# Kernel optimization log

Hardware: AMD Instinct MI355X
Metric: run time of the kernel (lower is better)

## Reference

```python
import jax, jax.numpy as jnp
import numpy as np
from jax import lax

SEQ, BATCH, IN, HID = 4096, 8, 1024, 1024


def setup_inputs() -> dict:
    key = jax.random.key(0)
    k1, k2 = jax.random.split(key)
    X = jax.random.normal(k1, (SEQ, BATCH, IN), dtype=jnp.float32)
    hidden = jnp.zeros((BATCH, HID), dtype=jnp.float32)  # None init == zeros
    W = jax.random.normal(k2, (3 * HID, IN), dtype=jnp.float32) * 0.02
    b = jnp.zeros((3 * HID,), dtype=jnp.float32)
    return {"X": X, "hidden": hidden, "W": W, "b": b}


def reference(X, hidden, W, b):
    # window=1: source = X; Y = Linear(X) -> [S, B, 3H]
    Y = jnp.einsum('sbi,hi->sbh', X, W) + b
    Z, F, O = jnp.split(Y, 3, axis=2)
    Z = jnp.tanh(Z)
    F = jax.nn.sigmoid(F)

    # ForgetMult: c_t = f_t * z_t + (1 - f_t) * c_{t-1}
    def step(c, fz):
        f, z = fz
        c = f * z + (1.0 - f) * c
        return c, c

    _, C = lax.scan(step, hidden, (F, Z))  # C: [S, B, H]
    H = jax.nn.sigmoid(O) * C
    return (H, C[-1:, :, :], C)
```

## Files before the change

### kernel.cpp

```cpp
#include <hip/hip_runtime.h>
#include <hip/hip_bf16.h>
#include <stdint.h>

#define S_   4096
#define B_   8
#define IN_  1024
#define H_   1024
#define M_   (S_ * B_)
#define N_   (3 * H_)
#define K_   IN_
#define CH_  (B_ * H_)
#define NC_  64
#define T_   (S_ / NC_)
#define STR8 (CH_ / 8)
#define STR4 (CH_ / 4)

typedef unsigned short u16;
typedef __bf16 bf16x8 __attribute__((ext_vector_type(8)));
typedef float  f32x4  __attribute__((ext_vector_type(4)));
typedef _Float16 h8   __attribute__((ext_vector_type(8)));

__device__ __forceinline__ u16 f2bf(float f) {
  unsigned u = __float_as_uint(f);
  u += 0x7fffu + ((u >> 16) & 1u);
  return (u16)(u >> 16);
}

__device__ __forceinline__ float sigmoid_(float x) { return 1.0f / (1.0f + __expf(-x)); }
__device__ __forceinline__ float tanh_(float x)    { return 2.0f / (1.0f + __expf(-2.0f * x)) - 1.0f; }

__global__ void cvt_all(const float* __restrict__ X, const float* __restrict__ W,
                        u16* __restrict__ Xb, u16* __restrict__ Wb) {
  const int nX = M_ * K_ / 8, nW = N_ * K_ / 8;
  int i = blockIdx.x * blockDim.x + threadIdx.x;
  const float* in; u16* out; int j;
  if (i < nX)           { in = X; out = Xb; j = i; }
  else if (i < nX + nW) { in = W; out = Wb; j = i - nX; }
  else return;
  const float4* p = (const float4*)in;
  float4 a = p[2 * j], b = p[2 * j + 1];
  alignas(16) u16 us[8] = {f2bf(a.x), f2bf(a.y), f2bf(a.z), f2bf(a.w),
                           f2bf(b.x), f2bf(b.y), f2bf(b.z), f2bf(b.w)};
  ((uint4*)out)[j] = *(const uint4*)us;
}

#define SWZ(x) ((x) ^ (((x) >> 3) & 0x30))

#define DS_A(s, h, mh) do {                                                    \
  const char* base_ = (const char*)As_[(s)*2+(h)];                             \
  af[0] = *(const bf16x8*)(base_ + aoff[mh][0]);                               \
  af[1] = *(const bf16x8*)(base_ + aoff[mh][1]);                               \
  af[2] = *(const bf16x8*)(base_ + aoff[mh][2]);                               \
  af[3] = *(const bf16x8*)(base_ + aoff[mh][3]);                               \
} while (0)

#define DS_B(s, h) do {                                                        \
  const char* base_ = (const char*)Bs_[(s)*2+(h)];                             \
  bfr[0] = *(const bf16x8*)(base_ + boff[0]);                                  \
  bfr[1] = *(const bf16x8*)(base_ + boff[1]);                                  \
  bfr[2] = *(const bf16x8*)(base_ + boff[2]);                                  \
  bfr[3] = *(const bf16x8*)(base_ + boff[3]);                                  \
} while (0)

#define MMA(mh) do {                                                           \
  __builtin_amdgcn_s_setprio(1);                                              \
  _Pragma("unroll")                                                            \
  for (int fi_ = 0; fi_ < 4; ++fi_)                                            \
    _Pragma("unroll")                                                          \
    for (int fj_ = 0; fj_ < 4; ++fj_)                                          \
      acc[(mh)*4+fi_][fj_] = __builtin_amdgcn_mfma_f32_16x16x32_bf16(          \
          af[fi_], bfr[fj_], acc[(mh)*4+fi_][fj_], 0, 0, 0);                   \
  __builtin_amdgcn_s_setprio(0);                                              \
} while (0)

#define PH_SYNC() do {                                                         \
  asm volatile("" ::: "memory");                                               \
  __builtin_amdgcn_s_barrier();                                                \
  asm volatile("s_waitcnt lgkmcnt(0)" ::: "memory");                           \
} while (0)

#define PH_END() do {                                                          \
  asm volatile("" ::: "memory");                                               \
  __builtin_amdgcn_s_barrier();                                                \
} while (0)

#define VW(n) asm volatile("s_waitcnt vmcnt(" #n ")" ::: "memory")

__global__ __launch_bounds__(512, 2) void gemm_act(
    const u16* __restrict__ Ab, const u16* __restrict__ Bb,
    const float* __restrict__ bias,
    _Float16* __restrict__ zh,
    _Float16* __restrict__ fh,
    float* __restrict__ Ho) {
  __shared__ alignas(16) u16 As_[4][8192];
  __shared__ alignas(16) u16 Bs_[4][8192];

  const int tid = threadIdx.x;
  const int w = tid >> 6, l = tid & 63;
  const int m0 = blockIdx.y * 256, n0 = blockIdx.x * 256;
  const int wmo = (w >> 2) * 128, wno = (w & 3) * 64;
  const int lr = l & 15, lq = l >> 4;

  const int D0b  = w * 1024 + l * 16;
  const int row0 = D0b >> 6;
  const int c0   = (SWZ(D0b) & 63) >> 1;

  int aoff[2][4], boff[4];
#pragma unroll
  for (int mh = 0; mh < 2; ++mh)
#pragma unroll
    for (int fi = 0; fi < 4; ++fi)
      aoff[mh][fi] = SWZ((wmo + (mh * 4 + fi) * 16 + lr) * 64 + lq * 16);
#pragma unroll
  for (int fj = 0; fj < 4; ++fj)
    boff[fj] = SWZ((wno + fj * 16 + lr) * 64 + lq * 16);

  auto stage = [&](const u16* __restrict__ G, int rb, int tt, int hh, u16* dstp) {
    const u16* s0 = G + (size_t)(rb + row0) * K_ + (tt * 64 + hh * 32 + c0);
    __builtin_amdgcn_global_load_lds(
        (const __attribute__((address_space(1))) void*)s0,
        (__attribute__((address_space(3))) void*)(dstp + (D0b >> 1)), 16, 0, 0);
    const u16* s1 = s0 + (size_t)128 * K_;
    __builtin_amdgcn_global_load_lds(
        (const __attribute__((address_space(1))) void*)s1,
        (__attribute__((address_space(3))) void*)(dstp + (D0b >> 1) + 4096), 16, 0, 0);
  };

  f32x4 acc[8][4] = {};
  bf16x8 af[4], bfr[4];

  stage(Ab, m0, 0, 0, As_[0]); stage(Bb, n0, 0, 0, Bs_[0]);
  stage(Ab, m0, 0, 1, As_[1]); stage(Bb, n0, 0, 1, Bs_[1]);
  stage(Ab, m0, 1, 0, As_[2]); stage(Bb, n0, 1, 0, Bs_[2]);
  VW(4);
  PH_END();

  for (int i = 0; i < 7; ++i) {
    const int t1 = 2 * i + 1, t2 = 2 * i + 2, t3 = 2 * i + 3;
    DS_A(0, 0, 0); DS_B(0, 0); stage(Ab, m0, t1, 1, As_[3]);
    PH_SYNC(); MMA(0); PH_END();
    DS_A(0, 0, 1);             stage(Bb, n0, t1, 1, Bs_[3]);
    PH_SYNC(); MMA(1); PH_END();
    DS_A(0, 1, 0); DS_B(0, 1); stage(Ab, m0, t2, 0, As_[0]);
    PH_SYNC(); MMA(0); PH_END();
    DS_A(0, 1, 1);             stage(Bb, n0, t2, 0, Bs_[0]); VW(4);
    PH_SYNC(); MMA(1); PH_END();
    DS_A(1, 0, 0); DS_B(1, 0); stage(Ab, m0, t2, 1, As_[1]);
    PH_SYNC(); MMA(0); PH_END();
    DS_A(1, 0, 1);             stage(Bb, n0, t2, 1, Bs_[1]);
    PH_SYNC(); MMA(1); PH_END();
    DS_A(1, 1, 0); DS_B(1, 1); stage(Ab, m0, t3, 0, As_[2]);
    PH_SYNC(); MMA(0); PH_END();
    DS_A(1, 1, 1);             stage(Bb, n0, t3, 0, Bs_[2]); VW(4);
    PH_SYNC(); MMA(1); PH_END();
  }

  DS_A(0, 0, 0); DS_B(0, 0); stage(Ab, m0, 15, 1, As_[3]);
  PH_SYNC(); MMA(0); PH_END();
  DS_A(0, 0, 1);             stage(Bb, n0, 15, 1, Bs_[3]);
  PH_SYNC(); MMA(1); PH_END();
  DS_A(0, 1, 0); DS_B(0, 1);
  PH_SYNC(); MMA(0); PH_END();
  DS_A(0, 1, 1); VW(0);
  PH_SYNC(); MMA(1); PH_END();
  DS_A(1, 0, 0); DS_B(1, 0);
  PH_SYNC(); MMA(0); PH_END();
  DS_A(1, 0, 1);
  PH_SYNC(); MMA(1); PH_END();
  DS_A(1, 1, 0); DS_B(1, 1);
  PH_SYNC(); MMA(0); PH_END();
  DS_A(1, 1, 1);
  PH_SYNC(); MMA(1); PH_END();

  const int seg = n0 >> 10;
  const int nh0 = (n0 & 1023) + wno;
#pragma unroll
  for (int fj = 0; fj < 4; ++fj) {
    const int nn = nh0 + fj * 16 + lr;
    const float bv = bias[seg * 1024 + nn];
#pragma unroll
    for (int fi = 0; fi < 8; ++fi) {
#pragma unroll
      for (int rr = 0; rr < 4; ++rr) {
        const int mm = m0 + wmo + fi * 16 + lq * 4 + rr;
        const float v = acc[fi][fj][rr] + bv;
        const size_t idx = (size_t)mm * H_ + nn;
        if (seg == 0)      zh[idx] = (_Float16)tanh_(v);
        else if (seg == 1) fh[idx] = (_Float16)sigmoid_(v);
        else               Ho[idx] = sigmoid_(v);
      }
    }
  }
}


__global__ void scanA(const _Float16* __restrict__ fhp, const _Float16* __restrict__ zhp,
                      float* __restrict__ ckA, float* __restrict__ ckC) {
  const int ch8 = blockIdx.x * 256 + threadIdx.x;
  const int j   = blockIdx.y;
  const h8* __restrict__ fh = (const h8*)fhp;
  const h8* __restrict__ zh = (const h8*)zhp;
  size_t base = (size_t)j * T_ * STR8 + ch8;
  float A[8], c[8];
#pragma unroll
  for (int k = 0; k < 8; ++k) { A[k] = 1.f; c[k] = 0.f; }
  h8 f0 = fh[base],        z0 = zh[base];
  h8 f1 = fh[base + STR8], z1 = zh[base + STR8];
  for (int tt = 0; tt < T_ - 2; ++tt) {
    const h8 f2 = fh[base + 2 * STR8];
    const h8 z2 = zh[base + 2 * STR8];
#pragma unroll
    for (int k = 0; k < 8; ++k) {
      const float f = (float)f0[k], z = (float)z0[k], om = 1.f - f;
      c[k] = f * z + om * c[k]; A[k] *= om;
    }
    f0 = f1; z0 = z1; f1 = f2; z1 = z2; base += STR8;
  }
#pragma unroll
  for (int k = 0; k < 8; ++k) {
    const float f = (float)f0[k], z = (float)z0[k], om = 1.f - f;
    c[k] = f * z + om * c[k]; A[k] *= om;
  }
#pragma unroll
  for (int k = 0; k < 8; ++k) {
    const float f = (float)f1[k], z = (float)z1[k], om = 1.f - f;
    c[k] = f * z + om * c[k]; A[k] *= om;
  }
  float4* a4 = (float4*)ckA; float4* c4 = (float4*)ckC;
  const size_t o4 = (size_t)j * STR4 + ch8 * 2;
  a4[o4]     = float4{A[0], A[1], A[2], A[3]};
  a4[o4 + 1] = float4{A[4], A[5], A[6], A[7]};
  c4[o4]     = float4{c[0], c[1], c[2], c[3]};
  c4[o4 + 1] = float4{c[4], c[5], c[6], c[7]};
}

__global__ void scanComb(const float* __restrict__ ckA, const float* __restrict__ ckC,
                         const float* __restrict__ hidden, float* __restrict__ carry) {
  const int ch4 = blockIdx.x * 64 + threadIdx.x;
  const float4* __restrict__ a4 = (const float4*)ckA;
  const float4* __restrict__ c4 = (const float4*)ckC;
  float4* __restrict__ cr4 = (float4*)carry;
  float4 c = ((const float4*)hidden)[ch4];
  float4 A0 = a4[ch4], C0 = c4[ch4];
#pragma unroll 8
  for (int j = 0; j < NC_ - 1; ++j) {
    const float4 A1 = a4[(size_t)(j + 1) * STR4 + ch4];
    const float4 C1 = c4[(size_t)(j + 1) * STR4 + ch4];
    cr4[(size_t)j * STR4 + ch4] = c;
    c.x = C0.x + A0.x * c.x;
    c.y = C0.y + A0.y * c.y;
    c.z = C0.z + A0.z * c.z;
    c.w = C0.w + A0.w * c.w;
    A0 = A1; C0 = C1;
  }
  cr4[(size_t)(NC_ - 1) * STR4 + ch4] = c;
}

__global__ void scanB(const _Float16* __restrict__ fhp, const _Float16* __restrict__ zhp,
                      float* __restrict__ Cw,
                      float* __restrict__ Ho,
                      float* __restrict__ Clast,
                      const float* __restrict__ carry) {
  const int ch8 = blockIdx.x * 256 + threadIdx.x;
  const int j   = blockIdx.y;
  const h8* __restrict__ fh = (const h8*)fhp;
  const h8* __restrict__ zh = (const h8*)zhp;
  float4* __restrict__ H4 = (float4*)Ho;
  float4* __restrict__ C4 = (float4*)Cw;
  size_t b8 = (size_t)j * T_ * STR8 + ch8;
  size_t b4 = (size_t)j * T_ * STR4 + ch8 * 2;
  const float4 ca = ((const float4*)carry)[(size_t)j * STR4 + ch8 * 2];
  const float4 cb = ((const float4*)carry)[(size_t)j * STR4 + ch8 * 2 + 1];
  float c[8] = {ca.x, ca.y, ca.z, ca.w, cb.x, cb.y, cb.z, cb.w};
  h8 f0 = fh[b8],        z0 = zh[b8];
  float4 oa0 = H4[b4], ob0 = H4[b4 + 1];
  h8 f1 = fh[b8 + STR8], z1 = zh[b8 + STR8];
  float4 oa1 = H4[b4 + STR4], ob1 = H4[b4 + STR4 + 1];
  for (int tt = 0; tt < T_ - 2; ++tt) {
    const h8 f2 = fh[b8 + 2 * STR8];
    const h8 z2 = zh[b8 + 2 * STR8];
    const float4 oa2 = H4[b4 + 2 * STR4], ob2 = H4[b4 + 2 * STR4 + 1];
#pragma unroll
    for (int k = 0; k < 8; ++k) {
      const float f = (float)f0[k], z = (float)z0[k];
      c[k] = f * z + (1.f - f) * c[k];
    }
    C4[b4]     = float4{c[0], c[1], c[2], c[3]};
    C4[b4 + 1] = float4{c[4], c[5], c[6], c[7]};
    H4[b4]     = float4{oa0.x * c[0], oa0.y * c[1], oa0.z * c[2], oa0.w * c[3]};
    H4[b4 + 1] = float4{ob0.x * c[4], ob0.y * c[5], ob0.z * c[6], ob0.w * c[7]};
    f0 = f1; z0 = z1; oa0 = oa1; ob0 = ob1;
    f1 = f2; z1 = z2; oa1 = oa2; ob1 = ob2;
    b8 += STR8; b4 += STR4;
  }
#pragma unroll
  for (int k = 0; k < 8; ++k) {
    const float f = (float)f0[k], z = (float)z0[k];
    c[k] = f * z + (1.f - f) * c[k];
  }
  C4[b4]     = float4{c[0], c[1], c[2], c[3]};
  C4[b4 + 1] = float4{c[4], c[5], c[6], c[7]};
  H4[b4]     = float4{oa0.x * c[0], oa0.y * c[1], oa0.z * c[2], oa0.w * c[3]};
  H4[b4 + 1] = float4{ob0.x * c[4], ob0.y * c[5], ob0.z * c[6], ob0.w * c[7]};
  b4 += STR4;
#pragma unroll
  for (int k = 0; k < 8; ++k) {
    const float f = (float)f1[k], z = (float)z1[k];
    c[k] = f * z + (1.f - f) * c[k];
  }
  C4[b4]     = float4{c[0], c[1], c[2], c[3]};
  C4[b4 + 1] = float4{c[4], c[5], c[6], c[7]};
  H4[b4]     = float4{oa1.x * c[0], oa1.y * c[1], oa1.z * c[2], oa1.w * c[3]};
  H4[b4 + 1] = float4{ob1.x * c[4], ob1.y * c[5], ob1.z * c[6], ob1.w * c[7]};
  if (j == NC_ - 1) {
    ((float4*)Clast)[ch8 * 2]     = float4{c[0], c[1], c[2], c[3]};
    ((float4*)Clast)[ch8 * 2 + 1] = float4{c[4], c[5], c[6], c[7]};
  }
}

extern "C" void kernel_launch(void* const* d_in, const int* in_sizes, int n_in,
                              void* d_out, int out_size, void* d_ws, size_t ws_size,
                              hipStream_t stream) {
  const float* X    = (const float*)d_in[0];
  const float* hid  = (const float*)d_in[1];
  const float* W    = (const float*)d_in[2];
  const float* bias = (const float*)d_in[3];

  float* out   = (float*)d_out;
  float* Ho    = out;
  float* Clast = out + (size_t)M_ * H_;
  float* Cf    = Clast + CH_;

  char* ws = (char*)d_ws;
  u16*      Xb  = (u16*)ws;
  u16*      Wb  = (u16*)(ws + 67108864);
  _Float16* zh  = (_Float16*)(ws + 73400320);
  _Float16* fhg = (_Float16*)(ws + 140509184);
  float* ckA    = (float*)(ws + 207618048);
  float* ckC    = (float*)(ws + 209715200);
  float* carry  = (float*)(ws + 211812352);

  const int nAll = M_ * K_ / 8 + N_ * K_ / 8;
  cvt_all<<<(nAll + 255) / 256, 256, 0, stream>>>(X, W, Xb, Wb);
  gemm_act<<<dim3(N_ / 256, M_ / 256), 512, 0, stream>>>(Xb, Wb, bias, zh, fhg, Ho);
  scanA<<<dim3(CH_ / 8 / 256, NC_), 256, 0, stream>>>(fhg, zh, ckA, ckC);
  scanComb<<<CH_ / 4 / 64, 64, 0, stream>>>(ckA, ckC, hid, carry);
  scanB<<<dim3(CH_ / 8 / 256, NC_), 256, 0, stream>>>(fhg, zh, Cf, Ho, Clast, carry);
}
```

Before: 770.4 us.

## Fuse scan phases with flag-based chunk carry and interleave z/f in LDS-staged layout

Merges the three scan kernels into one fused_scan kernel. Each chunk block publishes its local decay and carry products, then waits on per-chunk flags and recomputes its incoming carry serially from earlier chunks, which removes two kernel launches and the carry buffer. The GEMM epilogue now stages tanh/sigmoid outputs through LDS and writes z and f interleaved per row with wide stores, so the scan reads them from one contiguous region. The cost is spin-waiting that assumes all 256 blocks are co-resident, plus an O(j) carry recompute per block.

```diff
diff --git a/kernel.cpp b/kernel.cpp
--- a/kernel.cpp
+++ b/kernel.cpp
@@ -12,8 +12,6 @@
 #define CH_  (B_ * H_)
 #define NC_  64
 #define T_   (S_ / NC_)
-#define STR8 (CH_ / 8)
-#define STR4 (CH_ / 4)
 
 typedef unsigned short u16;
 typedef __bf16 bf16x8 __attribute__((ext_vector_type(8)));
@@ -30,7 +28,9 @@
 __device__ __forceinline__ float tanh_(float x)    { return 2.0f / (1.0f + __expf(-2.0f * x)) - 1.0f; }
 
 __global__ void cvt_all(const float* __restrict__ X, const float* __restrict__ W,
-                        u16* __restrict__ Xb, u16* __restrict__ Wb) {
+                        u16* __restrict__ Xb, u16* __restrict__ Wb,
+                        unsigned* __restrict__ flags) {
+  if (blockIdx.x == 0 && threadIdx.x < 256) flags[threadIdx.x] = 0;
   const int nX = M_ * K_ / 8, nW = N_ * K_ / 8;
   int i = blockIdx.x * blockDim.x + threadIdx.x;
   const float* in; u16* out; int j;
@@ -89,8 +89,7 @@
 __global__ __launch_bounds__(512, 2) void gemm_act(
     const u16* __restrict__ Ab, const u16* __restrict__ Bb,
     const float* __restrict__ bias,
-    _Float16* __restrict__ zh,
-    _Float16* __restrict__ fh,
+    _Float16* __restrict__ G,
     float* __restrict__ Ho) {
   __shared__ alignas(16) u16 As_[4][8192];
   __shared__ alignas(16) u16 Bs_[4][8192];
@@ -115,8 +114,8 @@
   for (int fj = 0; fj < 4; ++fj)
     boff[fj] = SWZ((wno + fj * 16 + lr) * 64 + lq * 16);
 
-  auto stage = [&](const u16* __restrict__ G, int rb, int tt, int hh, u16* dstp) {
-    const u16* s0 = G + (size_t)(rb + row0) * K_ + (tt * 64 + hh * 32 + c0);
+  auto stage = [&](const u16* __restrict__ Gg, int rb, int tt, int hh, u16* dstp) {
+    const u16* s0 = Gg + (size_t)(rb + row0) * K_ + (tt * 64 + hh * 32 + c0);
     __builtin_amdgcn_global_load_lds(
         (const __attribute__((address_space(1))) void*)s0,
         (__attribute__((address_space(3))) void*)(dstp + (D0b >> 1)), 16, 0, 0);
@@ -173,48 +172,84 @@
   PH_SYNC(); MMA(1); PH_END();
 
   const int seg = n0 >> 10;
-  const int nh0 = (n0 & 1023) + wno;
-#pragma unroll
-  for (int fj = 0; fj < 4; ++fj) {
-    const int nn = nh0 + fj * 16 + lr;
-    const float bv = bias[seg * 1024 + nn];
-#pragma unroll
-    for (int fi = 0; fi < 8; ++fi) {
-#pragma unroll
-      for (int rr = 0; rr < 4; ++rr) {
-        const int mm = m0 + wmo + fi * 16 + lq * 4 + rr;
-        const float v = acc[fi][fj][rr] + bv;
-        const size_t idx = (size_t)mm * H_ + nn;
-        if (seg == 0)      zh[idx] = (_Float16)tanh_(v);
-        else if (seg == 1) fh[idx] = (_Float16)sigmoid_(v);
-        else               Ho[idx] = sigmoid_(v);
+  if (seg == 2) {
+    const int nh0 = (n0 & 1023) + wno;
+#pragma unroll
+    for (int fj = 0; fj < 4; ++fj) {
+      const int nn = nh0 + fj * 16 + lr;
+      const float bv = bias[2048 + nn];
+#pragma unroll
+      for (int fi = 0; fi < 8; ++fi) {
+#pragma unroll
+        for (int rr = 0; rr < 4; ++rr) {
+          const int mm = m0 + wmo + fi * 16 + lq * 4 + rr;
+          Ho[(size_t)mm * H_ + nn] = sigmoid_(acc[fi][fj][rr] + bv);
+        }
       }
     }
-  }
-}
-
-
-__global__ void scanA(const _Float16* __restrict__ fhp, const _Float16* __restrict__ zhp,
-                      float* __restrict__ ckA, float* __restrict__ ckC) {
-  const int ch8 = blockIdx.x * 256 + threadIdx.x;
-  const int j   = blockIdx.y;
-  const h8* __restrict__ fh = (const h8*)fhp;
-  const h8* __restrict__ zh = (const h8*)zhp;
-  size_t base = (size_t)j * T_ * STR8 + ch8;
+  } else {
+    _Float16* myhalf = (_Float16*)((wmo == 0) ? (u16*)As_ : (u16*)Bs_);
+#pragma unroll
+    for (int fj = 0; fj < 4; ++fj) {
+      const int col = wno + fj * 16 + lr;
+      const float bv = bias[seg * 1024 + (n0 & 1023) + col];
+#pragma unroll
+      for (int fi = 0; fi < 8; ++fi) {
+#pragma unroll
+        for (int rr = 0; rr < 4; ++rr) {
+          const int row = wmo + fi * 16 + lq * 4 + rr;
+          const float v = acc[fi][fj][rr] + bv;
+          const float av = (seg == 0) ? tanh_(v) : sigmoid_(v);
+          const int off = ((row & 127) << 9) + ((col * 2) ^ ((row & 15) << 4));
+          *(_Float16*)((char*)myhalf + off) = (_Float16)av;
+        }
+      }
+    }
+    __syncthreads();
+    const int chk = tid & 31;
+#pragma unroll
+    for (int k = 0; k < 16; ++k) {
+      const int row = (tid >> 5) + k * 16;
+      const char* half_ = (const char*)((row < 128) ? (u16*)As_ : (u16*)Bs_);
+      const h8 v = *(const h8*)(half_ + ((row & 127) << 9) +
+                                ((chk * 16) ^ ((row & 15) << 4)));
+      const size_t dsth8 = (size_t)(m0 + row) * 256 + seg * 128 +
+                           ((n0 & 1023) >> 3) + chk;
+      ((h8*)G)[dsth8] = v;
+    }
+  }
+}
+
+__global__ __launch_bounds__(256) void fused_scan(
+    const _Float16* __restrict__ G,
+    float* __restrict__ Ho,
+    float* __restrict__ Cw,
+    float* __restrict__ Clast,
+    const float* __restrict__ hidden,
+    float* __restrict__ ckA, float* __restrict__ ckC,
+    unsigned* __restrict__ flags) {
+  const int x = blockIdx.x, j = blockIdx.y;
+  const int tid = threadIdx.x;
+  const int ch8 = x * 256 + tid;
+  const int b = ch8 >> 7, hh = ch8 & 127;
+  const h8* __restrict__ G8 = (const h8*)G;
+  const size_t STEP = 2048;
+
   float A[8], c[8];
 #pragma unroll
   for (int k = 0; k < 8; ++k) { A[k] = 1.f; c[k] = 0.f; }
-  h8 f0 = fh[base],        z0 = zh[base];
-  h8 f1 = fh[base + STR8], z1 = zh[base + STR8];
+  size_t base = ((size_t)j * T_ * 8 + b) * 256 + hh;
+  h8 z0 = G8[base],        f0 = G8[base + 128];
+  h8 z1 = G8[base + STEP], f1 = G8[base + STEP + 128];
   for (int tt = 0; tt < T_ - 2; ++tt) {
-    const h8 f2 = fh[base + 2 * STR8];
-    const h8 z2 = zh[base + 2 * STR8];
+    const h8 z2 = G8[base + 2 * STEP];
+    const h8 f2 = G8[base + 2 * STEP + 128];
 #pragma unroll
     for (int k = 0; k < 8; ++k) {
       const float f = (float)f0[k], z = (float)z0[k], om = 1.f - f;
       c[k] = f * z + om * c[k]; A[k] *= om;
     }
-    f0 = f1; z0 = z1; f1 = f2; z1 = z2; base += STR8;
+    f0 = f1; z0 = z1; f1 = f2; z1 = z2; base += STEP;
   }
 #pragma unroll
   for (int k = 0; k < 8; ++k) {
@@ -226,60 +261,62 @@
     const float f = (float)f1[k], z = (float)z1[k], om = 1.f - f;
     c[k] = f * z + om * c[k]; A[k] *= om;
   }
-  float4* a4 = (float4*)ckA; float4* c4 = (float4*)ckC;
-  const size_t o4 = (size_t)j * STR4 + ch8 * 2;
-  a4[o4]     = float4{A[0], A[1], A[2], A[3]};
-  a4[o4 + 1] = float4{A[4], A[5], A[6], A[7]};
-  c4[o4]     = float4{c[0], c[1], c[2], c[3]};
-  c4[o4 + 1] = float4{c[4], c[5], c[6], c[7]};
-}
-
-__global__ void scanComb(const float* __restrict__ ckA, const float* __restrict__ ckC,
-                         const float* __restrict__ hidden, float* __restrict__ carry) {
-  const int ch4 = blockIdx.x * 64 + threadIdx.x;
-  const float4* __restrict__ a4 = (const float4*)ckA;
-  const float4* __restrict__ c4 = (const float4*)ckC;
-  float4* __restrict__ cr4 = (float4*)carry;
-  float4 c = ((const float4*)hidden)[ch4];
-  float4 A0 = a4[ch4], C0 = c4[ch4];
-#pragma unroll 8
-  for (int j = 0; j < NC_ - 1; ++j) {
-    const float4 A1 = a4[(size_t)(j + 1) * STR4 + ch4];
-    const float4 C1 = c4[(size_t)(j + 1) * STR4 + ch4];
-    cr4[(size_t)j * STR4 + ch4] = c;
-    c.x = C0.x + A0.x * c.x;
-    c.y = C0.y + A0.y * c.y;
-    c.z = C0.z + A0.z * c.z;
-    c.w = C0.w + A0.w * c.w;
-    A0 = A1; C0 = C1;
-  }
-  cr4[(size_t)(NC_ - 1) * STR4 + ch4] = c;
-}
-
-__global__ void scanB(const _Float16* __restrict__ fhp, const _Float16* __restrict__ zhp,
-                      float* __restrict__ Cw,
-                      float* __restrict__ Ho,
-                      float* __restrict__ Clast,
-                      const float* __restrict__ carry) {
-  const int ch8 = blockIdx.x * 256 + threadIdx.x;
-  const int j   = blockIdx.y;
-  const h8* __restrict__ fh = (const h8*)fhp;
-  const h8* __restrict__ zh = (const h8*)zhp;
+  {
+    float4* a4 = (float4*)ckA; float4* c4 = (float4*)ckC;
+    const size_t o4 = (size_t)j * STEP + ch8 * 2;
+    a4[o4]     = float4{A[0], A[1], A[2], A[3]};
+    a4[o4 + 1] = float4{A[4], A[5], A[6], A[7]};
+    c4[o4]     = float4{c[0], c[1], c[2], c[3]};
+    c4[o4 + 1] = float4{c[4], c[5], c[6], c[7]};
+  }
+  __syncthreads();
+  __threadfence();
+  if (tid == 0)
+    __hip_atomic_store(&flags[x * 64 + j], 1u, __ATOMIC_RELEASE,
+                       __HIP_MEMORY_SCOPE_AGENT);
+
+  if (tid < j) {
+    while (__hip_atomic_load(&flags[x * 64 + tid], __ATOMIC_ACQUIRE,
+                             __HIP_MEMORY_SCOPE_AGENT) == 0u)
+      __builtin_amdgcn_s_sleep(2);
+  }
+  __syncthreads();
+
+  float cin[8];
+  {
+    const float4 ha = ((const float4*)hidden)[ch8 * 2];
+    const float4 hb = ((const float4*)hidden)[ch8 * 2 + 1];
+    cin[0]=ha.x; cin[1]=ha.y; cin[2]=ha.z; cin[3]=ha.w;
+    cin[4]=hb.x; cin[5]=hb.y; cin[6]=hb.z; cin[7]=hb.w;
+  }
+  {
+    const float4* a4 = (const float4*)ckA;
+    const float4* c4 = (const float4*)ckC;
+    for (int i = 0; i < j; ++i) {
+      const size_t o4 = (size_t)i * STEP + ch8 * 2;
+      const float4 Aa = a4[o4], Ab = a4[o4 + 1];
+      const float4 Ca = c4[o4], Cb = c4[o4 + 1];
+      cin[0] = Ca.x + Aa.x * cin[0]; cin[1] = Ca.y + Aa.y * cin[1];
+      cin[2] = Ca.z + Aa.z * cin[2]; cin[3] = Ca.w + Aa.w * cin[3];
+      cin[4] = Cb.x + Ab.x * cin[4]; cin[5] = Cb.y + Ab.y * cin[5];
+      cin[6] = Cb.z + Ab.z * cin[6]; cin[7] = Cb.w + Ab.w * cin[7];
+    }
+  }
+
+#pragma unroll
+  for (int k = 0; k < 8; ++k) c[k] = cin[k];
+  base = ((size_t)j * T_ * 8 + b) * 256 + hh;
+  size_t b4 = ((size_t)j * T_ * 8 + b) * 256 + hh * 2;
   float4* __restrict__ H4 = (float4*)Ho;
   float4* __restrict__ C4 = (float4*)Cw;
-  size_t b8 = (size_t)j * T_ * STR8 + ch8;
-  size_t b4 = (size_t)j * T_ * STR4 + ch8 * 2;
-  const float4 ca = ((const float4*)carry)[(size_t)j * STR4 + ch8 * 2];
-  const float4 cb = ((const float4*)carry)[(size_t)j * STR4 + ch8 * 2 + 1];
-  float c[8] = {ca.x, ca.y, ca.z, ca.w, cb.x, cb.y, cb.z, cb.w};
-  h8 f0 = fh[b8],        z0 = zh[b8];
+  z0 = G8[base];        f0 = G8[base + 128];
+  z1 = G8[base + STEP]; f1 = G8[base + STEP + 128];
   float4 oa0 = H4[b4], ob0 = H4[b4 + 1];
-  h8 f1 = fh[b8 + STR8], z1 = zh[b8 + STR8];
-  float4 oa1 = H4[b4 + STR4], ob1 = H4[b4 + STR4 + 1];
+  float4 oa1 = H4[b4 + STEP], ob1 = H4[b4 + STEP + 1];
   for (int tt = 0; tt < T_ - 2; ++tt) {
-    const h8 f2 = fh[b8 + 2 * STR8];
-    const h8 z2 = zh[b8 + 2 * STR8];
-    const float4 oa2 = H4[b4 + 2 * STR4], ob2 = H4[b4 + 2 * STR4 + 1];
+    const h8 z2 = G8[base + 2 * STEP];
+    const h8 f2 = G8[base + 2 * STEP + 128];
+    const float4 oa2 = H4[b4 + 2 * STEP], ob2 = H4[b4 + 2 * STEP + 1];
 #pragma unroll
     for (int k = 0; k < 8; ++k) {
       const float f = (float)f0[k], z = (float)z0[k];
@@ -291,7 +328,7 @@
     H4[b4 + 1] = float4{ob0.x * c[4], ob0.y * c[5], ob0.z * c[6], ob0.w * c[7]};
     f0 = f1; z0 = z1; oa0 = oa1; ob0 = ob1;
     f1 = f2; z1 = z2; oa1 = oa2; ob1 = ob2;
-    b8 += STR8; b4 += STR4;
+    base += STEP; b4 += STEP;
   }
 #pragma unroll
   for (int k = 0; k < 8; ++k) {
@@ -302,7 +339,7 @@
   C4[b4 + 1] = float4{c[4], c[5], c[6], c[7]};
   H4[b4]     = float4{oa0.x * c[0], oa0.y * c[1], oa0.z * c[2], oa0.w * c[3]};
   H4[b4 + 1] = float4{ob0.x * c[4], ob0.y * c[5], ob0.z * c[6], ob0.w * c[7]};
-  b4 += STR4;
+  b4 += STEP;
 #pragma unroll
   for (int k = 0; k < 8; ++k) {
     const float f = (float)f1[k], z = (float)z1[k];
@@ -332,18 +369,16 @@
   float* Cf    = Clast + CH_;
 
   char* ws = (char*)d_ws;
-  u16*      Xb  = (u16*)ws;
-  u16*      Wb  = (u16*)(ws + 67108864);
-  _Float16* zh  = (_Float16*)(ws + 73400320);
-  _Float16* fhg = (_Float16*)(ws + 140509184);
-  float* ckA    = (float*)(ws + 207618048);
-  float* ckC    = (float*)(ws + 209715200);
-  float* carry  = (float*)(ws + 211812352);
+  u16*      Xb   = (u16*)ws;
+  u16*      Wb   = (u16*)(ws + 67108864);
+  _Float16* Gh   = (_Float16*)(ws + 73400320);
+  float*    ckA  = (float*)(ws + 207618048);
+  float*    ckC  = (float*)(ws + 209715200);
+  unsigned* flags= (unsigned*)(ws + 211812352);
 
   const int nAll = M_ * K_ / 8 + N_ * K_ / 8;
-  cvt_all<<<(nAll + 255) / 256, 256, 0, stream>>>(X, W, Xb, Wb);
-  gemm_act<<<dim3(N_ / 256, M_ / 256), 512, 0, stream>>>(Xb, Wb, bias, zh, fhg, Ho);
-  scanA<<<dim3(CH_ / 8 / 256, NC_), 256, 0, stream>>>(fhg, zh, ckA, ckC);
-  scanComb<<<CH_ / 4 / 64, 64, 0, stream>>>(ckA, ckC, hid, carry);
-  scanB<<<dim3(CH_ / 8 / 256, NC_), 256, 0, stream>>>(fhg, zh, Cf, Ho, Clast, carry);
-}
+  cvt_all<<<(nAll + 255) / 256, 256, 0, stream>>>(X, W, Xb, Wb, flags);
+  gemm_act<<<dim3(N_ / 256, M_ / 256), 512, 0, stream>>>(Xb, Wb, bias, Gh, Ho);
+  fused_scan<<<dim3(4, NC_), 256, 0, stream>>>(Gh, Ho, Cf, Clast, hid,
+                                               ckA, ckC, flags);
+}
```

Result: slower. 810.7 us (+5.2%).
